# Kernel tuning notes

Measured on AMD Instinct MI355X. Metric: run time of the kernel, lower is better.

The kernel has to match this reference:

```python
import jax, jax.numpy as jnp
import numpy as np

C = 1.0                 # ball curvature magnitude (k = -c)
SQRT_C = float(np.sqrt(C))
MIN_NORM = 1e-15
BALL_EPS = 4e-3         # geoopt float32 projection eps


def _artanh(x):
    return jnp.arctanh(jnp.clip(x, -1.0 + 1e-7, 1.0 - 1e-7))


def _norm(x):
    return jnp.clip(jnp.linalg.norm(x, axis=-1, keepdims=True), MIN_NORM)


def expmap0(u):
    n = _norm(u)
    return jnp.tanh(SQRT_C * n) * u / (SQRT_C * n)


def logmap0(y):
    n = _norm(y)
    return _artanh(SQRT_C * n) * y / (SQRT_C * n)


def mobius_add(x, y):
    x2 = jnp.sum(x * x, axis=-1, keepdims=True)
    y2 = jnp.sum(y * y, axis=-1, keepdims=True)
    xy = jnp.sum(x * y, axis=-1, keepdims=True)
    num = (1.0 + 2.0 * C * xy + C * y2) * x + (1.0 - C * x2) * y
    den = 1.0 + 2.0 * C * xy + C * C * x2 * y2
    return num / jnp.clip(den, MIN_NORM)


def mobius_matvec(W, x):
    # x: [N, in], W: [out, in]
    mx = x @ W.T                                   # [N, out]
    xn = _norm(x)
    mxn = _norm(mx)
    res = jnp.tanh(mxn / xn * _artanh(SQRT_C * xn)) * mx / (mxn * SQRT_C)
    zero = jnp.linalg.norm(mx, axis=-1, keepdims=True) <= 1e-10
    return jnp.where(zero, jnp.zeros_like(res), res)


def project(x):
    n = _norm(x)
    maxnorm = (1.0 - BALL_EPS) / SQRT_C
    return jnp.where(n > maxnorm, x * (maxnorm / n), x)


def setup_inputs() -> dict:
    key = jax.random.key(0)
    k1, k2, k3, k4, k5 = jax.random.split(key, 5)
    N, E, D_IN, D_OUT = 100000, 600000, 128, 128
    x_h = jax.random.normal(k1, (N, D_IN), dtype=jnp.float32) * 0.05  # inside ball
    edge_index = jax.random.randint(k2, (2, E), 0, N, dtype=jnp.int64)
    edge_weight = jax.random.uniform(k3, (E,), dtype=jnp.float32)
    xav = float(np.sqrt(2.0 / (D_IN + D_OUT)))
    W = jax.random.normal(k4, (D_OUT, D_IN), dtype=jnp.float32) * xav
    b = jax.random.normal(k5, (D_OUT,), dtype=jnp.float32) * 0.01
    a = jnp.asarray(0.25, dtype=jnp.float32)  # PReLU slope
    return {"x_h": x_h, "edge_index": edge_index, "edge_weight": edge_weight,
            "W": W, "b": b, "a": a}


def reference(x_h, edge_index, edge_weight, W, b, a):
    N = x_h.shape[0]
    # HyperbolicLinear: mobius matvec + mobius bias add
    h = mobius_matvec(W, x_h)
    h = mobius_add(h, expmap0(b))
    # tangent-space aggregation
    h_t = logmap0(h)                                  # [N, D]
    src, dst = edge_index[0], edge_index[1]
    msg = h_t[src] * edge_weight[:, None]             # [E, D]
    agg = jax.ops.segment_sum(msg, dst, num_segments=N) + h_t
    # mobius PReLU activation
    h2_t = logmap0(expmap0(agg))
    h2_t = jnp.where(h2_t >= 0, h2_t, a * h2_t)
    return project(expmap0(h2_t))
```

## Files before the change

kernel.cpp:

```cpp
#include <hip/hip_runtime.h>
#include <hip/hip_fp16.h>
#include <cstdint>

#define D 128
#define BLK 256

constexpr float MINN    = 1e-15f;
constexpr float ATCLIP  = 1.0f - 1e-7f;
constexpr float BALLEPS = 4e-3f;

typedef _Float16 f16x8 __attribute__((ext_vector_type(8)));
typedef float    f32x4 __attribute__((ext_vector_type(4)));

union H4 { _Float16 h[4]; uint2 u2; };
union H8 { _Float16 h[8]; uint4 u4; };

typedef __attribute__((address_space(1))) const void gas_v;
typedef __attribute__((address_space(3))) void las_v;

__device__ __forceinline__ float red64(float v) {
    v += __shfl_xor(v, 1, 64);
    v += __shfl_xor(v, 2, 64);
    v += __shfl_xor(v, 4, 64);
    v += __shfl_xor(v, 8, 64);
    v += __shfl_xor(v, 16, 64);
    v += __shfl_xor(v, 32, 64);
    return v;
}

__device__ __forceinline__ float red16(float v) {
    v += __shfl_xor(v, 1, 64);
    v += __shfl_xor(v, 2, 64);
    v += __shfl_xor(v, 4, 64);
    v += __shfl_xor(v, 8, 64);
    return v;
}

__device__ __forceinline__ float tanh_fast(float x) {
    float e = __expf(2.f * fminf(x, 15.f));
    return __fdividef(e - 1.f, e + 1.f);
}
__device__ __forceinline__ float artanh_fast(float x) {
    x = fminf(x, ATCLIP);
    return 0.5f * __logf(__fdividef(1.f + x, 1.f - x));
}

__global__ __launch_bounds__(256) void k_prep(const float* __restrict__ W,
                                              _Float16* __restrict__ Wh,
                                              int* __restrict__ cnt, int N)
{
    const int t = threadIdx.x;
    const int bid = blockIdx.x;
    if (bid < 8) {
        int i = bid * 256 + t;
        int f = i >> 7;
        int r = i & 127;
        const float4* src = (const float4*)(W + r * 128 + f * 8);
        float4 v0 = src[0], v1 = src[1];
        H8 u;
        u.h[0] = (_Float16)v0.x; u.h[1] = (_Float16)v0.y;
        u.h[2] = (_Float16)v0.z; u.h[3] = (_Float16)v0.w;
        u.h[4] = (_Float16)v1.x; u.h[5] = (_Float16)v1.y;
        u.h[6] = (_Float16)v1.z; u.h[7] = (_Float16)v1.w;
        *(uint4*)(Wh + i * 8) = u.u4;
    } else {
        int i = (bid - 8) * 256 + t;
        int base = i * 4;
        if (base + 3 < N) {
            *(int4*)(cnt + base) = make_int4(0, 0, 0, 0);
        } else if (base < N) {
            for (int k = base; k < N; ++k) cnt[k] = 0;
        }
    }
}

__global__ __launch_bounds__(BLK) void k_node_mfma(
    const float* __restrict__ x, const _Float16* __restrict__ Wh,
    const float* __restrict__ b, uint2* __restrict__ ht, int N,
    const int* __restrict__ ei, int* __restrict__ cnt,
    int* __restrict__ rank, int E, int eslice, int use_rank)
{
    __shared__ float xs[64 * 128];

    const int t     = threadIdx.x;
    const int node0 = blockIdx.x * 64;
    const int lane  = t & 63;
    const int w     = t >> 6;

#pragma unroll
    for (int i = 0; i < 8; ++i) {
        int P      = (w * 8 + i) * 64 + lane;
        int node   = P >> 5;
        int q      = (P & 31) ^ (node & 7);
        int node_g = min(node0 + node, N - 1);
        const float* src = x + (size_t)node_g * 128 + q * 4;
        char* dst = (char*)xs + (size_t)(w * 8 + i) * 1024;
        __builtin_amdgcn_global_load_lds((gas_v*)src, (las_v*)dst, 16, 0, 0);
    }

    float2 b2 = ((const float2*)b)[lane];
    float pb  = fmaf(b2.x, b2.x, b2.y * b2.y);
    float bn2 = red64(pb);
    float bnc    = fmaxf(sqrtf(bn2), MINN);
    float bscale = __fdividef(tanh_fast(bnc), bnc);
    const float y2 = bscale * bscale * bn2;
    __syncthreads();

    const int c = lane & 15;
    const int g = lane >> 4;

    f32x4 Cf[8];
#pragma unroll
    for (int mt = 0; mt < 8; ++mt) Cf[mt] = (f32x4){0.f, 0.f, 0.f, 0.f};

    const int bnode = w * 16 + c;
    const int sw    = bnode & 7;
    const float* xrow = &xs[bnode * 128];
    float px = 0.f;

#pragma unroll
    for (int s = 0; s < 4; ++s) {
        int q0 = s * 8 + g * 2;
        f32x4 lo = *(const f32x4*)&xrow[(q0 ^ sw) * 4];
        f32x4 hi = *(const f32x4*)&xrow[((q0 + 1) ^ sw) * 4];
        px = fmaf(lo[0], lo[0], px); px = fmaf(lo[1], lo[1], px);
        px = fmaf(lo[2], lo[2], px); px = fmaf(lo[3], lo[3], px);
        px = fmaf(hi[0], hi[0], px); px = fmaf(hi[1], hi[1], px);
        px = fmaf(hi[2], hi[2], px); px = fmaf(hi[3], hi[3], px);
        f16x8 Bf;
        Bf[0] = (_Float16)lo[0]; Bf[1] = (_Float16)lo[1];
        Bf[2] = (_Float16)lo[2]; Bf[3] = (_Float16)lo[3];
        Bf[4] = (_Float16)hi[0]; Bf[5] = (_Float16)hi[1];
        Bf[6] = (_Float16)hi[2]; Bf[7] = (_Float16)hi[3];
        const _Float16* wp = Wh + ((s * 4 + g) << 10) + (c << 3);
#pragma unroll
        for (int mt = 0; mt < 8; ++mt) {
            f16x8 Af = *(const f16x8*)&wp[mt << 7];
            Cf[mt] = __builtin_amdgcn_mfma_f32_16x16x32_f16(Af, Bf, Cf[mt], 0, 0, 0);
        }
    }

    const float4* b4 = (const float4*)b;
    float pm = 0.f, pdb = 0.f;
#pragma unroll
    for (int mt = 0; mt < 8; ++mt) {
        float4 bv = b4[mt * 4 + g];
        pm  = fmaf(Cf[mt][0], Cf[mt][0], pm);
        pm  = fmaf(Cf[mt][1], Cf[mt][1], pm);
        pm  = fmaf(Cf[mt][2], Cf[mt][2], pm);
        pm  = fmaf(Cf[mt][3], Cf[mt][3], pm);
        pdb = fmaf(Cf[mt][0], bv.x, pdb);
        pdb = fmaf(Cf[mt][1], bv.y, pdb);
        pdb = fmaf(Cf[mt][2], bv.z, pdb);
        pdb = fmaf(Cf[mt][3], bv.w, pdb);
    }
    float xn2 = px;
    xn2 += __shfl_xor(xn2, 16); xn2 += __shfl_xor(xn2, 32);
    pm  += __shfl_xor(pm, 16);  pm  += __shfl_xor(pm, 32);
    pdb += __shfl_xor(pdb, 16); pdb += __shfl_xor(pdb, 32);
    float pd = bscale * pdb;

    float xn      = fmaxf(sqrtf(xn2), MINN);
    float mxn_raw = sqrtf(pm);
    float mxn     = fmaxf(mxn_raw, MINN);
    float alpha   = __fdividef(tanh_fast(__fdividef(mxn, xn) * artanh_fast(xn)), mxn);
    if (mxn_raw <= 1e-10f) alpha = 0.f;

    float x2  = alpha * alpha * pm;
    float xy  = alpha * pd;
    float den = fmaxf(fmaf(x2, y2, 1.f + 2.f * xy), MINN);
    float ca  = __fdividef((1.f + 2.f * xy + y2) * alpha, den);
    float cb  = __fdividef(1.f - x2, den);

    float hn2 = ca * ca * pm + 2.f * ca * cb * pd + cb * cb * y2;
    float hn  = fmaxf(sqrtf(hn2), MINN);
    float lsc = __fdividef(artanh_fast(hn), hn);
    float s1  = lsc * ca;
    float s2b = lsc * cb * bscale;

    uint2* lout = (uint2*)((char*)xs + (size_t)w * 8192);
#pragma unroll
    for (int mt = 0; mt < 8; ++mt) {
        float4 bv = b4[mt * 4 + g];
        H4 u;
        u.h[0] = (_Float16)fmaf(s1, Cf[mt][0], s2b * bv.x);
        u.h[1] = (_Float16)fmaf(s1, Cf[mt][1], s2b * bv.y);
        u.h[2] = (_Float16)fmaf(s1, Cf[mt][2], s2b * bv.z);
        u.h[3] = (_Float16)fmaf(s1, Cf[mt][3], s2b * bv.w);
        lout[c * 33 + mt * 4 + g] = u.u2;
    }
    __syncthreads();

    for (int it = 0; it < 8; ++it) {
        int lin  = it * BLK + t;
        int node = lin >> 5;
        int col  = lin & 31;
        int gn   = node0 + node;
        if (gn < N) {
            const uint2* lsrc = (const uint2*)((const char*)xs + (size_t)(node >> 4) * 8192);
            ht[(size_t)gn * 32 + col] = lsrc[(node & 15) * 33 + col];
        }
    }

    {
        int e0 = blockIdx.x * eslice;
        if (use_rank) {
            for (int i = t; i < eslice; i += BLK) {
                int e = e0 + i;
                if (e < E) rank[e] = atomicAdd(&cnt[ei[E + e]], 1);
            }
        } else {
            for (int i = t; i < eslice; i += BLK) {
                int e = e0 + i;
                if (e < E) atomicAdd(&cnt[ei[E + e]], 1);
            }
        }
    }
}

__global__ __launch_bounds__(256) void k_scan1(
    const int* __restrict__ cnt, int* __restrict__ ptr,
    int* __restrict__ part, int N)
{
    __shared__ int s[256];
    int t = threadIdx.x;
    int base = blockIdx.x * 1024 + t * 4;
    int v0 = 0, v1 = 0, v2 = 0, v3 = 0;
    if (base + 3 < N) {
        int4 q = *(const int4*)&cnt[base];
        v0 = q.x; v1 = q.y; v2 = q.z; v3 = q.w;
    } else {
        if (base + 0 < N) v0 = cnt[base + 0];
        if (base + 1 < N) v1 = cnt[base + 1];
        if (base + 2 < N) v2 = cnt[base + 2];
        if (base + 3 < N) v3 = cnt[base + 3];
    }
    int sum = v0 + v1 + v2 + v3;
    s[t] = sum;
    __syncthreads();
    for (int off = 1; off < 256; off <<= 1) {
        int xv = (t >= off) ? s[t - off] : 0;
        __syncthreads();
        s[t] += xv;
        __syncthreads();
    }
    int excl = s[t] - sum;
    if (t == 255) part[blockIdx.x] = s[255];
    int r = excl;
    if (base + 0 < N) ptr[base + 0] = r; r += v0;
    if (base + 1 < N) ptr[base + 1] = r; r += v1;
    if (base + 2 < N) ptr[base + 2] = r; r += v2;
    if (base + 3 < N) ptr[base + 3] = r;
}

__global__ __launch_bounds__(256) void k_scan2(int* __restrict__ part, int nc) {
    __shared__ int s[256];
    int t = threadIdx.x;
    int v = (t < nc) ? part[t] : 0;
    s[t] = v;
    __syncthreads();
    for (int off = 1; off < 256; off <<= 1) {
        int xv = (t >= off) ? s[t - off] : 0;
        __syncthreads();
        s[t] += xv;
        __syncthreads();
    }
    if (t < nc) part[t] = s[t] - v;
}

__global__ __launch_bounds__(256) void k_scatter_rank(
    const int* __restrict__ ei, const float* __restrict__ ew,
    const int* __restrict__ ptr, const int* __restrict__ part,
    const int* __restrict__ rank, int2* __restrict__ sorted, int E)
{
    int e = blockIdx.x * 256 + threadIdx.x;
    if (e >= E) return;
    int src = ei[e];
    int dst = ei[E + e];
    float w = ew[e];
    int pos = ptr[dst] + part[dst >> 10] + rank[e];
    sorted[pos] = make_int2(src << 8, __float_as_int(w));
}

__global__ __launch_bounds__(256) void k_scatter_atomic(
    const int* __restrict__ ei, const float* __restrict__ ew,
    int* __restrict__ ptr, const int* __restrict__ part,
    int2* __restrict__ sorted, int E)
{
    int e = blockIdx.x * 256 + threadIdx.x;
    if (e >= E) return;
    int src = ei[e];
    int dst = ei[E + e];
    float w = ew[e];
    int pos = atomicAdd(&ptr[dst], 1) + part[dst >> 10];
    sorted[pos] = make_int2(src << 8, __float_as_int(w));
}

__global__ __launch_bounds__(256) void k_agg_final(
    const char* __restrict__ htb, const int* __restrict__ ptr,
    const int* __restrict__ part, const int* __restrict__ cnt,
    const int2* __restrict__ sorted, const float* __restrict__ a_in,
    float* __restrict__ out, int N, int rmode)
{
    const int t   = threadIdx.x;
    const int li  = t & 15;
    const int grp = t >> 4;
    const int n   = blockIdx.x * 16 + grp;
    if (n >= N) return;
    const float a = a_in[0];

    H8 own; own.u4 = *(const uint4*)(htb + (size_t)n * 256 + li * 16);
    float acc[8];
#pragma unroll
    for (int k = 0; k < 8; ++k) acc[k] = (float)own.h[k];

    int basep = ptr[n] + part[n >> 10];
    int cn    = cnt[n];
    int s0    = rmode ? basep : basep - cn;
    int e0    = s0 + cn;

    const int lioff = li * 16;
    int j = s0;
    for (; j + 2 <= e0; j += 2) {
        int2 d0 = sorted[j];
        int2 d1 = sorted[j + 1];
        H8 g0, g1;
        g0.u4 = *(const uint4*)(htb + (unsigned)d0.x + lioff);
        g1.u4 = *(const uint4*)(htb + (unsigned)d1.x + lioff);
        float w0 = __int_as_float(d0.y);
        float w1 = __int_as_float(d1.y);
#pragma unroll
        for (int k = 0; k < 8; ++k) acc[k] = fmaf((float)g0.h[k], w0, acc[k]);
#pragma unroll
        for (int k = 0; k < 8; ++k) acc[k] = fmaf((float)g1.h[k], w1, acc[k]);
    }
    if (j < e0) {
        int2 d = sorted[j];
        H8 g; g.u4 = *(const uint4*)(htb + (unsigned)d.x + lioff);
        float w = __int_as_float(d.y);
#pragma unroll
        for (int k = 0; k < 8; ++k) acc[k] = fmaf((float)g.h[k], w, acc[k]);
    }

    float pv = 0.f;
#pragma unroll
    for (int k = 0; k < 8; ++k) {
        float v = acc[k];
        v = (v >= 0.f) ? v : a * v;
        acc[k] = v;
        pv = fmaf(v, v, pv);
    }
    float m2 = red16(pv);
    float rc = fmaxf(sqrtf(m2), MINN);
    float te = tanh_fast(rc);
    const float maxn = 1.0f - BALLEPS;
    float fsc = __fdividef(fminf(fmaxf(te, MINN), maxn), rc);

    float4 o0 = make_float4(fsc * acc[0], fsc * acc[1], fsc * acc[2], fsc * acc[3]);
    float4 o1 = make_float4(fsc * acc[4], fsc * acc[5], fsc * acc[6], fsc * acc[7]);
    float4* orow = (float4*)(out + (size_t)n * D);
    orow[li * 2 + 0] = o0;
    orow[li * 2 + 1] = o1;
}

extern "C" void kernel_launch(void* const* d_in, const int* in_sizes, int n_in,
                              void* d_out, int out_size, void* d_ws, size_t ws_size,
                              hipStream_t stream)
{
    const float* x  = (const float*)d_in[0];
    const int*   ei = (const int*)  d_in[1];
    const float* ew = (const float*)d_in[2];
    const float* W  = (const float*)d_in[3];
    const float* b  = (const float*)d_in[4];
    const float* a  = (const float*)d_in[5];
    float* out = (float*)d_out;

    const int N = in_sizes[0] / D;
    const int E = in_sizes[1] / 2;

    char* ws = (char*)d_ws;
    size_t HT_B    = (size_t)N * D * 2;
    uint2*     ht     = (uint2*)ws;
    int*       cnt    = (int*)(ws + HT_B);
    int*       ptr    = (int*)(ws + HT_B + (size_t)N * 4);
    int*       part   = (int*)(ws + HT_B + (size_t)N * 8);
    int2*      sorted = (int2*)(ws + HT_B + (size_t)N * 8 + 1024);
    _Float16*  Wh     = (_Float16*)(ws + HT_B + (size_t)N * 8 + 1024 + (size_t)E * 8);
    size_t base_end   = HT_B + (size_t)N * 8 + 1024 + (size_t)E * 8 + 32768;
    int*       rank   = (int*)(ws + base_end);
    int use_rank = (ws_size >= base_end + (size_t)E * 4) ? 1 : 0;

    int nc  = (N + 1023) / 1024;
    int nb1 = (N + 63) / 64;
    int eslice = (E + nb1 - 1) / nb1;
    int zb  = (((N + 3) / 4) + 255) / 256;

    k_prep<<<8 + zb, 256, 0, stream>>>(W, Wh, cnt, N);
    k_node_mfma<<<nb1, BLK, 0, stream>>>(x, Wh, b, ht, N, ei, cnt,
                                         use_rank ? rank : nullptr, E, eslice, use_rank);
    k_scan1<<<nc, 256, 0, stream>>>(cnt, ptr, part, N);
    k_scan2<<<1, 256, 0, stream>>>(part, nc);
    if (use_rank)
        k_scatter_rank<<<(E + 255) / 256, 256, 0, stream>>>(ei, ew, ptr, part, rank, sorted, E);
    else
        k_scatter_atomic<<<(E + 255) / 256, 256, 0, stream>>>(ei, ew, ptr, part, sorted, E);
    k_agg_final<<<(N + 15) / 16, 256, 0, stream>>>((const char*)ht, ptr, part, cnt, sorted, a, out, N, use_rank);
}
```

Measured before the change: 191.9 us.

## Use single-pass decoupled look-back scan and drop LDS staging in node kernel

Replaces the two-kernel prefix scan (block scan plus a single-block scan of partials) with one kernel that uses decoupled look-back over per-block flag/value packets, so ptr already holds global offsets and the part array lookups disappear downstream. The node MFMA kernel now loads x rows directly from global memory into registers and writes ht directly, instead of staging through LDS with async loads and barriers. This removes one launch and extra indirections, at the risk of spin-waiting blocks and less coalesced direct global loads and stores.

```diff
diff --git a/kernel.cpp b/kernel.cpp
--- a/kernel.cpp
+++ b/kernel.cpp
@@ -14,9 +14,6 @@
 
 union H4 { _Float16 h[4]; uint2 u2; };
 union H8 { _Float16 h[8]; uint4 u4; };
-
-typedef __attribute__((address_space(1))) const void gas_v;
-typedef __attribute__((address_space(3))) void las_v;
 
 __device__ __forceinline__ float red64(float v) {
     v += __shfl_xor(v, 1, 64);
@@ -28,6 +25,16 @@
     return v;
 }
 
+__device__ __forceinline__ int red64i(int v) {
+    v += __shfl_xor(v, 1, 64);
+    v += __shfl_xor(v, 2, 64);
+    v += __shfl_xor(v, 4, 64);
+    v += __shfl_xor(v, 8, 64);
+    v += __shfl_xor(v, 16, 64);
+    v += __shfl_xor(v, 32, 64);
+    return v;
+}
+
 __device__ __forceinline__ float red16(float v) {
     v += __shfl_xor(v, 1, 64);
     v += __shfl_xor(v, 2, 64);
@@ -47,7 +54,7 @@
 
 __global__ __launch_bounds__(256) void k_prep(const float* __restrict__ W,
                                               _Float16* __restrict__ Wh,
-                                              int* __restrict__ cnt, int N)
+                                              int* __restrict__ zero, int zeroInts)
 {
     const int t = threadIdx.x;
     const int bid = blockIdx.x;
@@ -66,10 +73,10 @@
     } else {
         int i = (bid - 8) * 256 + t;
         int base = i * 4;
-        if (base + 3 < N) {
-            *(int4*)(cnt + base) = make_int4(0, 0, 0, 0);
-        } else if (base < N) {
-            for (int k = base; k < N; ++k) cnt[k] = 0;
+        if (base + 3 < zeroInts) {
+            *(int4*)(zero + base) = make_int4(0, 0, 0, 0);
+        } else if (base < zeroInts) {
+            for (int k = base; k < zeroInts; ++k) zero[k] = 0;
         }
     }
 }
@@ -80,23 +87,10 @@
     const int* __restrict__ ei, int* __restrict__ cnt,
     int* __restrict__ rank, int E, int eslice, int use_rank)
 {
-    __shared__ float xs[64 * 128];
-
     const int t     = threadIdx.x;
     const int node0 = blockIdx.x * 64;
     const int lane  = t & 63;
     const int w     = t >> 6;
-
-#pragma unroll
-    for (int i = 0; i < 8; ++i) {
-        int P      = (w * 8 + i) * 64 + lane;
-        int node   = P >> 5;
-        int q      = (P & 31) ^ (node & 7);
-        int node_g = min(node0 + node, N - 1);
-        const float* src = x + (size_t)node_g * 128 + q * 4;
-        char* dst = (char*)xs + (size_t)(w * 8 + i) * 1024;
-        __builtin_amdgcn_global_load_lds((gas_v*)src, (las_v*)dst, 16, 0, 0);
-    }
 
     float2 b2 = ((const float2*)b)[lane];
     float pb  = fmaf(b2.x, b2.x, b2.y * b2.y);
@@ -104,39 +98,47 @@
     float bnc    = fmaxf(sqrtf(bn2), MINN);
     float bscale = __fdividef(tanh_fast(bnc), bnc);
     const float y2 = bscale * bscale * bn2;
-    __syncthreads();
 
     const int c = lane & 15;
     const int g = lane >> 4;
-
-    f32x4 Cf[8];
-#pragma unroll
-    for (int mt = 0; mt < 8; ++mt) Cf[mt] = (f32x4){0.f, 0.f, 0.f, 0.f};
-
     const int bnode = w * 16 + c;
-    const int sw    = bnode & 7;
-    const float* xrow = &xs[bnode * 128];
+    const int gnode = node0 + bnode;
+    const int gcl   = min(gnode, N - 1);
+    const float* xrow = x + (size_t)gcl * 128;
+
+    f32x4 xv[8];
+#pragma unroll
+    for (int s = 0; s < 4; ++s) {
+        xv[2 * s]     = *(const f32x4*)&xrow[(s * 8 + g * 2) * 4];
+        xv[2 * s + 1] = *(const f32x4*)&xrow[(s * 8 + g * 2 + 1) * 4];
+    }
+
     float px = 0.f;
-
+    f16x8 Bf[4];
 #pragma unroll
     for (int s = 0; s < 4; ++s) {
-        int q0 = s * 8 + g * 2;
-        f32x4 lo = *(const f32x4*)&xrow[(q0 ^ sw) * 4];
-        f32x4 hi = *(const f32x4*)&xrow[((q0 + 1) ^ sw) * 4];
+        f32x4 lo = xv[2 * s], hi = xv[2 * s + 1];
         px = fmaf(lo[0], lo[0], px); px = fmaf(lo[1], lo[1], px);
         px = fmaf(lo[2], lo[2], px); px = fmaf(lo[3], lo[3], px);
         px = fmaf(hi[0], hi[0], px); px = fmaf(hi[1], hi[1], px);
         px = fmaf(hi[2], hi[2], px); px = fmaf(hi[3], hi[3], px);
-        f16x8 Bf;
-        Bf[0] = (_Float16)lo[0]; Bf[1] = (_Float16)lo[1];
-        Bf[2] = (_Float16)lo[2]; Bf[3] = (_Float16)lo[3];
-        Bf[4] = (_Float16)hi[0]; Bf[5] = (_Float16)hi[1];
-        Bf[6] = (_Float16)hi[2]; Bf[7] = (_Float16)hi[3];
+        Bf[s][0] = (_Float16)lo[0]; Bf[s][1] = (_Float16)lo[1];
+        Bf[s][2] = (_Float16)lo[2]; Bf[s][3] = (_Float16)lo[3];
+        Bf[s][4] = (_Float16)hi[0]; Bf[s][5] = (_Float16)hi[1];
+        Bf[s][6] = (_Float16)hi[2]; Bf[s][7] = (_Float16)hi[3];
+    }
+
+    f32x4 Cf[8];
+#pragma unroll
+    for (int mt = 0; mt < 8; ++mt) Cf[mt] = (f32x4){0.f, 0.f, 0.f, 0.f};
+
+#pragma unroll
+    for (int s = 0; s < 4; ++s) {
         const _Float16* wp = Wh + ((s * 4 + g) << 10) + (c << 3);
 #pragma unroll
         for (int mt = 0; mt < 8; ++mt) {
             f16x8 Af = *(const f16x8*)&wp[mt << 7];
-            Cf[mt] = __builtin_amdgcn_mfma_f32_16x16x32_f16(Af, Bf, Cf[mt], 0, 0, 0);
+            Cf[mt] = __builtin_amdgcn_mfma_f32_16x16x32_f16(Af, Bf[s], Cf[mt], 0, 0, 0);
         }
     }
 
@@ -178,27 +180,17 @@
     float s1  = lsc * ca;
     float s2b = lsc * cb * bscale;
 
-    uint2* lout = (uint2*)((char*)xs + (size_t)w * 8192);
-#pragma unroll
-    for (int mt = 0; mt < 8; ++mt) {
-        float4 bv = b4[mt * 4 + g];
-        H4 u;
-        u.h[0] = (_Float16)fmaf(s1, Cf[mt][0], s2b * bv.x);
-        u.h[1] = (_Float16)fmaf(s1, Cf[mt][1], s2b * bv.y);
-        u.h[2] = (_Float16)fmaf(s1, Cf[mt][2], s2b * bv.z);
-        u.h[3] = (_Float16)fmaf(s1, Cf[mt][3], s2b * bv.w);
-        lout[c * 33 + mt * 4 + g] = u.u2;
-    }
-    __syncthreads();
-
-    for (int it = 0; it < 8; ++it) {
-        int lin  = it * BLK + t;
-        int node = lin >> 5;
-        int col  = lin & 31;
-        int gn   = node0 + node;
-        if (gn < N) {
-            const uint2* lsrc = (const uint2*)((const char*)xs + (size_t)(node >> 4) * 8192);
-            ht[(size_t)gn * 32 + col] = lsrc[(node & 15) * 33 + col];
+    if (gnode < N) {
+        uint2* orow = ht + (size_t)gnode * 32;
+#pragma unroll
+        for (int mt = 0; mt < 8; ++mt) {
+            float4 bv = b4[mt * 4 + g];
+            H4 u;
+            u.h[0] = (_Float16)fmaf(s1, Cf[mt][0], s2b * bv.x);
+            u.h[1] = (_Float16)fmaf(s1, Cf[mt][1], s2b * bv.y);
+            u.h[2] = (_Float16)fmaf(s1, Cf[mt][2], s2b * bv.z);
+            u.h[3] = (_Float16)fmaf(s1, Cf[mt][3], s2b * bv.w);
+            orow[mt * 4 + g] = u.u2;
         }
     }
 
@@ -218,13 +210,18 @@
     }
 }
 
-__global__ __launch_bounds__(256) void k_scan1(
+__global__ __launch_bounds__(256) void k_scan(
     const int* __restrict__ cnt, int* __restrict__ ptr,
-    int* __restrict__ part, int N)
+    unsigned long long* __restrict__ lb, int N)
 {
     __shared__ int s[256];
-    int t = threadIdx.x;
-    int base = blockIdx.x * 1024 + t * 4;
+    __shared__ int sbase;
+    const int t   = threadIdx.x;
+    const int bid = blockIdx.x;
+    const int lane = t & 63;
+    const int w    = t >> 6;
+
+    int base = bid * 1024 + t * 4;
     int v0 = 0, v1 = 0, v2 = 0, v3 = 0;
     if (base + 3 < N) {
         int4 q = *(const int4*)&cnt[base];
@@ -244,63 +241,88 @@
         s[t] += xv;
         __syncthreads();
     }
-    int excl = s[t] - sum;
-    if (t == 255) part[blockIdx.x] = s[255];
-    int r = excl;
+    int excl  = s[t] - sum;
+    int total = s[255];
+
+    if (t == 255) {
+        unsigned long long pkt =
+            ((unsigned long long)((bid == 0) ? 2u : 1u) << 32) | (unsigned)total;
+        __hip_atomic_store(&lb[bid], pkt, __ATOMIC_RELEASE, __HIP_MEMORY_SCOPE_AGENT);
+        if (bid == 0) sbase = 0;
+    }
+
+    if (bid > 0 && w == 3) {
+        int exclb = 0;
+        int j = bid - 1;
+        while (true) {
+            int idx = j - lane;
+            unsigned f = 0; int v = 0;
+            if (idx >= 0) {
+                unsigned long long p;
+                do {
+                    p = __hip_atomic_load(&lb[idx], __ATOMIC_ACQUIRE, __HIP_MEMORY_SCOPE_AGENT);
+                    f = (unsigned)(p >> 32);
+                } while (f == 0);
+                v = (int)(unsigned)(p & 0xffffffffu);
+            }
+            unsigned long long m2 = __ballot(f == 2u);
+            if (m2) {
+                int Lstop = __ffsll((long long)m2) - 1;
+                int contrib = (lane <= Lstop) ? v : 0;
+                exclb += red64i(contrib);
+                break;
+            } else {
+                exclb += red64i((idx >= 0) ? v : 0);
+                j -= 64;
+            }
+        }
+        if (lane == 0) {
+            unsigned long long pkt2 =
+                ((unsigned long long)2u << 32) | (unsigned)(exclb + total);
+            __hip_atomic_store(&lb[bid], pkt2, __ATOMIC_RELEASE, __HIP_MEMORY_SCOPE_AGENT);
+            sbase = exclb;
+        }
+    }
+    __syncthreads();
+
+    int r = excl + sbase;
     if (base + 0 < N) ptr[base + 0] = r; r += v0;
     if (base + 1 < N) ptr[base + 1] = r; r += v1;
     if (base + 2 < N) ptr[base + 2] = r; r += v2;
     if (base + 3 < N) ptr[base + 3] = r;
 }
 
-__global__ __launch_bounds__(256) void k_scan2(int* __restrict__ part, int nc) {
-    __shared__ int s[256];
-    int t = threadIdx.x;
-    int v = (t < nc) ? part[t] : 0;
-    s[t] = v;
-    __syncthreads();
-    for (int off = 1; off < 256; off <<= 1) {
-        int xv = (t >= off) ? s[t - off] : 0;
-        __syncthreads();
-        s[t] += xv;
-        __syncthreads();
-    }
-    if (t < nc) part[t] = s[t] - v;
-}
-
 __global__ __launch_bounds__(256) void k_scatter_rank(
     const int* __restrict__ ei, const float* __restrict__ ew,
-    const int* __restrict__ ptr, const int* __restrict__ part,
-    const int* __restrict__ rank, int2* __restrict__ sorted, int E)
+    const int* __restrict__ ptr, const int* __restrict__ rank,
+    int2* __restrict__ sorted, int E)
 {
     int e = blockIdx.x * 256 + threadIdx.x;
     if (e >= E) return;
     int src = ei[e];
     int dst = ei[E + e];
     float w = ew[e];
-    int pos = ptr[dst] + part[dst >> 10] + rank[e];
+    int pos = ptr[dst] + rank[e];
     sorted[pos] = make_int2(src << 8, __float_as_int(w));
 }
 
 __global__ __launch_bounds__(256) void k_scatter_atomic(
     const int* __restrict__ ei, const float* __restrict__ ew,
-    int* __restrict__ ptr, const int* __restrict__ part,
-    int2* __restrict__ sorted, int E)
+    int* __restrict__ ptr, int2* __restrict__ sorted, int E)
 {
     int e = blockIdx.x * 256 + threadIdx.x;
     if (e >= E) return;
     int src = ei[e];
     int dst = ei[E + e];
     float w = ew[e];
-    int pos = atomicAdd(&ptr[dst], 1) + part[dst >> 10];
+    int pos = atomicAdd(&ptr[dst], 1);
     sorted[pos] = make_int2(src << 8, __float_as_int(w));
 }
 
 __global__ __launch_bounds__(256) void k_agg_final(
     const char* __restrict__ htb, const int* __restrict__ ptr,
-    const int* __restrict__ part, const int* __restrict__ cnt,
-    const int2* __restrict__ sorted, const float* __restrict__ a_in,
-    float* __restrict__ out, int N, int rmode)
+    const int* __restrict__ cnt, const int2* __restrict__ sorted,
+    const float* __restrict__ a_in, float* __restrict__ out, int N, int rmode)
 {
     const int t   = threadIdx.x;
     const int li  = t & 15;
@@ -314,7 +336,7 @@
 #pragma unroll
     for (int k = 0; k < 8; ++k) acc[k] = (float)own.h[k];
 
-    int basep = ptr[n] + part[n >> 10];
+    int basep = ptr[n];
     int cn    = cnt[n];
     int s0    = rmode ? basep : basep - cn;
     int e0    = s0 + cn;
@@ -377,32 +399,37 @@
 
     const int N = in_sizes[0] / D;
     const int E = in_sizes[1] / 2;
+    const int nc = (N + 1023) / 1024;
 
     char* ws = (char*)d_ws;
-    size_t HT_B    = (size_t)N * D * 2;
-    uint2*     ht     = (uint2*)ws;
-    int*       cnt    = (int*)(ws + HT_B);
-    int*       ptr    = (int*)(ws + HT_B + (size_t)N * 4);
-    int*       part   = (int*)(ws + HT_B + (size_t)N * 8);
-    int2*      sorted = (int2*)(ws + HT_B + (size_t)N * 8 + 1024);
-    _Float16*  Wh     = (_Float16*)(ws + HT_B + (size_t)N * 8 + 1024 + (size_t)E * 8);
-    size_t base_end   = HT_B + (size_t)N * 8 + 1024 + (size_t)E * 8 + 32768;
-    int*       rank   = (int*)(ws + base_end);
-    int use_rank = (ws_size >= base_end + (size_t)E * 4) ? 1 : 0;
-
-    int nc  = (N + 1023) / 1024;
+    size_t HT_B       = (size_t)N * D * 2;
+    uint2*              ht  = (uint2*)ws;
+    size_t off_cnt    = HT_B;
+    int*                cnt = (int*)(ws + off_cnt);
+    size_t off_lb     = (off_cnt + (size_t)N * 4 + 15) & ~(size_t)15;
+    unsigned long long* lb  = (unsigned long long*)(ws + off_lb);
+    size_t off_ptr    = (off_lb + (size_t)nc * 8 + 15) & ~(size_t)15;
+    int*                ptr = (int*)(ws + off_ptr);
+    size_t off_sorted = (off_ptr + (size_t)N * 4 + 15) & ~(size_t)15;
+    int2*               sorted = (int2*)(ws + off_sorted);
+    size_t off_wh     = off_sorted + (size_t)E * 8;
+    _Float16*           Wh  = (_Float16*)(ws + off_wh);
+    size_t off_rank   = off_wh + 32768;
+    int*                rank = (int*)(ws + off_rank);
+    int use_rank = (ws_size >= off_rank + (size_t)E * 4) ? 1 : 0;
+
+    int zeroInts = (int)((off_ptr - off_cnt) / 4);
+    int zb  = ((zeroInts + 3) / 4 + 255) / 256;
     int nb1 = (N + 63) / 64;
     int eslice = (E + nb1 - 1) / nb1;
-    int zb  = (((N + 3) / 4) + 255) / 256;
-
-    k_prep<<<8 + zb, 256, 0, stream>>>(W, Wh, cnt, N);
+
+    k_prep<<<8 + zb, 256, 0, stream>>>(W, Wh, cnt, zeroInts);
     k_node_mfma<<<nb1, BLK, 0, stream>>>(x, Wh, b, ht, N, ei, cnt,
                                          use_rank ? rank : nullptr, E, eslice, use_rank);
-    k_scan1<<<nc, 256, 0, stream>>>(cnt, ptr, part, N);
-    k_scan2<<<1, 256, 0, stream>>>(part, nc);
+    k_scan<<<nc, 256, 0, stream>>>(cnt, ptr, lb, N);
     if (use_rank)
-        k_scatter_rank<<<(E + 255) / 256, 256, 0, stream>>>(ei, ew, ptr, part, rank, sorted, E);
+        k_scatter_rank<<<(E + 255) / 256, 256, 0, stream>>>(ei, ew, ptr, rank, sorted, E);
     else
-        k_scatter_atomic<<<(E + 255) / 256, 256, 0, stream>>>(ei, ew, ptr, part, sorted, E);
-    k_agg_final<<<(N + 15) / 16, 256, 0, stream>>>((const char*)ht, ptr, part, cnt, sorted, a, out, N, use_rank);
-}
+        k_scatter_atomic<<<(E + 255) / 256, 256, 0, stream>>>(ei, ew, ptr, sorted, E);
+    k_agg_final<<<(N + 15) / 16, 256, 0, stream>>>((const char*)ht, ptr, cnt, sorted, a, out, N, use_rank);
+}
```

Measured after the change: 200.0 us. 4.2% more time.
